# Optimization experiments

Hardware: AMD Instinct MI355X
Metric: run time of the kernel (lower is better)

## Reference

```python
import jax, jax.numpy as jnp
import numpy as np

DT = 1.0            # neuron_config.base_config.dt (ms)
TAU_MEM = 10.0      # membrane time constant (ms)
SURROGATE_BETA = 1.0  # surrogate sigmoid sharpness for spike nonlinearity

B, P = 256, 4096


def setup_inputs() -> dict:
    key = jax.random.key(0)
    k1, k2, k3, k4 = jax.random.split(key, 4)
    return {
        "external_input": jax.random.normal(k1, (B, P), dtype=jnp.float32),
        "lateral_weights": jax.random.normal(k2, (P, P), dtype=jnp.float32) * 0.1,
        "population_activity": jax.random.uniform(k3, (P,), dtype=jnp.float32),
        "v": jax.random.normal(k4, (B, P), dtype=jnp.float32),
        "threshold": jnp.ones((B, P), dtype=jnp.float32),
    }


def reference(external_input, lateral_weights, population_activity, v, threshold):
    P_ = external_input.shape[1]
    # lateral inhibition: zero self-connections (inhibition_mask = eye == 0)
    masked_w = lateral_weights * (1.0 - jnp.eye(P_, dtype=lateral_weights.dtype))
    lateral = population_activity @ masked_w              # [P]
    total_input = external_input - lateral[None, :]        # [B, P]
    # vectorized adaptive-threshold LIF step across the whole population
    decay = jnp.exp(jnp.asarray(-DT / TAU_MEM, dtype=v.dtype))
    v_new = decay * v + total_input                        # [B, P]
    u = (v_new - threshold) / SURROGATE_BETA
    soft = jax.nn.sigmoid(u)
    hard = (v_new > threshold).astype(v.dtype)
    # straight-through spike: hard forward, sigmoid-surrogate gradient
    spikes = jax.lax.stop_gradient(hard - soft) + soft     # [B, P]
    return spikes
```

## Files before the change

kernel.cpp:

```cpp
#include <hip/hip_runtime.h>


#define PP 4096
#define BB 256

constexpr int ROWS_PER_CHUNK = 64;
constexpr int NCHUNK = PP / ROWS_PER_CHUNK;
constexpr int COLS_PER_TILE = 1024;
constexpr int NTILE = PP / COLS_PER_TILE;

__global__ __launch_bounds__(256)
void lateral_partial(const float* __restrict__ w, const float* __restrict__ pa,
                     double* __restrict__ part) {
    const int tile = blockIdx.x & (NTILE - 1);
    const int rch  = blockIdx.x >> 2;
    const int c    = tile * COLS_PER_TILE + (int)threadIdx.x * 4;
    const int r0   = rch * ROWS_PER_CHUNK;
    double a0 = 0.0, a1 = 0.0, a2 = 0.0, a3 = 0.0;
#pragma unroll 8
    for (int k = 0; k < ROWS_PER_CHUNK; ++k) {
        const int i = r0 + k;
        const double p = (double)pa[i];
        const float4 wv = *reinterpret_cast<const float4*>(w + (size_t)i * PP + c);
        a0 += (i == c + 0) ? 0.0 : p * (double)wv.x;
        a1 += (i == c + 1) ? 0.0 : p * (double)wv.y;
        a2 += (i == c + 2) ? 0.0 : p * (double)wv.z;
        a3 += (i == c + 3) ? 0.0 : p * (double)wv.w;
    }
    double* dst = part + (size_t)rch * PP + c;
    dst[0] = a0; dst[1] = a1; dst[2] = a2; dst[3] = a3;
}

__global__ __launch_bounds__(256)
void lateral_reduce(const double* __restrict__ part, double* __restrict__ lat) {
    const int j = blockIdx.x * 256 + (int)threadIdx.x;
    double s = 0.0;
#pragma unroll 8
    for (int r = 0; r < NCHUNK; ++r) s += part[(size_t)r * PP + j];
    lat[j] = s;
}

__global__ __launch_bounds__(256)
void spike(const float* __restrict__ ext, const float* __restrict__ v,
           const float* __restrict__ thr, const double* __restrict__ lat,
           float* __restrict__ out) {
    const size_t t = ((size_t)blockIdx.x * 256 + threadIdx.x) * 4;
    const int j = (int)(t & (PP - 1));
    const float4 e  = *reinterpret_cast<const float4*>(ext + t);
    const float4 vv = *reinterpret_cast<const float4*>(v + t);
    const float4 th = *reinterpret_cast<const float4*>(thr + t);
    const double l0 = lat[j], l1 = lat[j + 1], l2 = lat[j + 2], l3 = lat[j + 3];
    const double dec = 0.90483741803595952;
    float4 o;
    o.x = (dec * (double)vv.x + (double)e.x - l0 > (double)th.x) ? 1.0f : 0.0f;
    o.y = (dec * (double)vv.y + (double)e.y - l1 > (double)th.y) ? 1.0f : 0.0f;
    o.z = (dec * (double)vv.z + (double)e.z - l2 > (double)th.z) ? 1.0f : 0.0f;
    o.w = (dec * (double)vv.w + (double)e.w - l3 > (double)th.w) ? 1.0f : 0.0f;
    *reinterpret_cast<float4*>(out + t) = o;
}

extern "C" void kernel_launch(void* const* d_in, const int* in_sizes, int n_in,
                              void* d_out, int out_size, void* d_ws, size_t ws_size,
                              hipStream_t stream) {
    const float* ext = (const float*)d_in[0];
    const float* w   = (const float*)d_in[1];
    const float* pa  = (const float*)d_in[2];
    const float* v   = (const float*)d_in[3];
    const float* thr = (const float*)d_in[4];
    float* out = (float*)d_out;

    double* part = (double*)d_ws;
    double* lat  = part + (size_t)NCHUNK * PP;

    lateral_partial<<<NTILE * NCHUNK, 256, 0, stream>>>(w, pa, part);
    lateral_reduce<<<PP / 256, 256, 0, stream>>>(part, lat);
    spike<<<(BB * PP) / (4 * 256), 256, 0, stream>>>(ext, v, thr, lat, out);
}
```

Baseline: 118.3 us.

## Split lateral GEMV into finer row chunks and subtract diagonal in reduce

Cuts rows per chunk from 64 to 16, so the partial GEMV launches four times as many blocks and fills the GPU better. The per-element diagonal mask is dropped from the inner loop; the reduce kernel instead subtracts pa[j]*w[j][j] once per column. The reduce now splits the larger chunk count across four wavefront groups and combines them in shared memory, and partials are stored as double2. The partial buffer grows fourfold, adding workspace traffic and requiring more workspace memory.

```diff
diff --git a/kernel.cpp b/kernel.cpp
--- a/kernel.cpp
+++ b/kernel.cpp
@@ -4,7 +4,7 @@
 #define PP 4096
 #define BB 256
 
-constexpr int ROWS_PER_CHUNK = 64;
+constexpr int ROWS_PER_CHUNK = 16;
 constexpr int NCHUNK = PP / ROWS_PER_CHUNK;
 constexpr int COLS_PER_TILE = 1024;
 constexpr int NTILE = PP / COLS_PER_TILE;
@@ -17,27 +17,40 @@
     const int c    = tile * COLS_PER_TILE + (int)threadIdx.x * 4;
     const int r0   = rch * ROWS_PER_CHUNK;
     double a0 = 0.0, a1 = 0.0, a2 = 0.0, a3 = 0.0;
-#pragma unroll 8
+#pragma unroll
     for (int k = 0; k < ROWS_PER_CHUNK; ++k) {
         const int i = r0 + k;
         const double p = (double)pa[i];
         const float4 wv = *reinterpret_cast<const float4*>(w + (size_t)i * PP + c);
-        a0 += (i == c + 0) ? 0.0 : p * (double)wv.x;
-        a1 += (i == c + 1) ? 0.0 : p * (double)wv.y;
-        a2 += (i == c + 2) ? 0.0 : p * (double)wv.z;
-        a3 += (i == c + 3) ? 0.0 : p * (double)wv.w;
+        a0 += p * (double)wv.x;
+        a1 += p * (double)wv.y;
+        a2 += p * (double)wv.z;
+        a3 += p * (double)wv.w;
     }
     double* dst = part + (size_t)rch * PP + c;
-    dst[0] = a0; dst[1] = a1; dst[2] = a2; dst[3] = a3;
+    *reinterpret_cast<double2*>(dst)     = make_double2(a0, a1);
+    *reinterpret_cast<double2*>(dst + 2) = make_double2(a2, a3);
 }
 
 __global__ __launch_bounds__(256)
-void lateral_reduce(const double* __restrict__ part, double* __restrict__ lat) {
-    const int j = blockIdx.x * 256 + (int)threadIdx.x;
+void lateral_reduce(const double* __restrict__ part, const float* __restrict__ w,
+                    const float* __restrict__ pa, double* __restrict__ lat) {
+    __shared__ double sh[256];
+    const int lane = (int)threadIdx.x & 63;
+    const int grp  = (int)threadIdx.x >> 6;
+    const int col  = blockIdx.x * 64 + lane;
     double s = 0.0;
-#pragma unroll 8
-    for (int r = 0; r < NCHUNK; ++r) s += part[(size_t)r * PP + j];
-    lat[j] = s;
+    const int rbase = grp * (NCHUNK / 4);
+#pragma unroll 16
+    for (int r = 0; r < NCHUNK / 4; ++r)
+        s += part[(size_t)(rbase + r) * PP + col];
+    sh[threadIdx.x] = s;
+    __syncthreads();
+    if (grp == 0) {
+        double t = sh[lane] + sh[64 + lane] + sh[128 + lane] + sh[192 + lane];
+        t -= (double)pa[col] * (double)w[(size_t)col * (PP + 1)];
+        lat[col] = t;
+    }
 }
 
 __global__ __launch_bounds__(256)
@@ -73,6 +86,6 @@
     double* lat  = part + (size_t)NCHUNK * PP;
 
     lateral_partial<<<NTILE * NCHUNK, 256, 0, stream>>>(w, pa, part);
-    lateral_reduce<<<PP / 256, 256, 0, stream>>>(part, lat);
+    lateral_reduce<<<PP / 64, 256, 0, stream>>>(part, w, pa, lat);
     spike<<<(BB * PP) / (4 * 256), 256, 0, stream>>>(ext, v, thr, lat, out);
 }
```

Result: faster. 113.0 us (-4.5%).
